# Optimization experiments

Hardware: AMD Instinct MI355X
Metric: run time of the kernel (lower is better)

## Reference

```python
import jax, jax.numpy as jnp
import numpy as np

N_VISIBLE = 4096
N_HIDDEN = 4096
BATCH = 8192


def setup_inputs() -> dict:
    key = jax.random.key(0)
    k_x, k_w = jax.random.split(key)
    input_data = jax.random.uniform(k_x, (BATCH, N_VISIBLE), dtype=jnp.float32)
    # xavier_uniform with sigmoid gain (=1.0): limit = sqrt(6/(fan_in+fan_out))
    limit = float(np.sqrt(6.0 / (N_VISIBLE + N_HIDDEN)))
    W = jax.random.uniform(k_w, (N_VISIBLE, N_HIDDEN), dtype=jnp.float32,
                           minval=-limit, maxval=limit)
    hidden_bias = jnp.zeros((N_HIDDEN,), dtype=jnp.float32)
    return {"input_data": input_data, "W": W, "hidden_bias": hidden_bias}


def reference(input_data, W, hidden_bias):
    # RBM.sample_hidden_2 (forward): sigmoid(x @ W + b), batched over samples.
    # (The torch code loops per sample with host syncs; same math, vectorized.)
    hid_prob = jax.nn.sigmoid(jnp.matmul(input_data, W) + hidden_bias)
    return hid_prob
```

## Files before the change

kernel.cpp:

```cpp
#include <hip/hip_runtime.h>
#include <cstdint>

#define MDIM 8192
#define NDIM 4096
#define KDIM 4096
#define NT (KDIM / 64)

typedef __bf16 bf16x8 __attribute__((ext_vector_type(8)));
typedef float f32x4 __attribute__((ext_vector_type(4)));

#define MFMA16 __builtin_amdgcn_mfma_f32_16x16x32_bf16

__device__ __forceinline__ void gload_lds16(const void* g, void* l) {
    __builtin_amdgcn_global_load_lds(
        (const __attribute__((address_space(1))) uint32_t*)g,
        (__attribute__((address_space(3))) uint32_t*)l, 16, 0, 0);
}

__device__ __forceinline__ unsigned short bf16_bits(float f) {
    __bf16 b = (__bf16)f;
    return __builtin_bit_cast(unsigned short, b);
}

__device__ __forceinline__ int detect_f32(const void* X) {
    int ok = 1;
    if (threadIdx.x < 128) {
        unsigned short h = ((const unsigned short*)X)[threadIdx.x];
        ok = (h <= 0x3F80);
    }
    return __syncthreads_and(ok) ? 0 : 1;
}

__global__ __launch_bounds__(256) void prep(const void* __restrict__ X,
                                            const void* __restrict__ W,
                                            __bf16* __restrict__ Xb,
                                            __bf16* __restrict__ WT) {
    const int f32 = detect_f32(X);
    const int t = threadIdx.x;
    if (blockIdx.x < 8192) {
        if (!f32) return;
        const float* Xf = (const float*)X;
        const long xbase = (long)blockIdx.x * 4096;
#pragma unroll
        for (int rr = 0; rr < 4; ++rr) {
            const long idx = xbase + rr * 1024 + t * 4;
            float4 v = *(const float4*)(Xf + idx);
            unsigned short r[4] = {bf16_bits(v.x), bf16_bits(v.y),
                                   bf16_bits(v.z), bf16_bits(v.w)};
            *(uint2*)(Xb + idx) = *(const uint2*)r;
        }
        return;
    }
    __shared__ unsigned short tile[64 * 65];
    const int bid = blockIdx.x - 8192;
    const int n0 = (bid & 63) * 64;
    const int k0 = (bid >> 6) * 64;
    if (f32) {
        const float* Wf = (const float*)W;
#pragma unroll
        for (int p = 0; p < 4; ++p) {
            const int ch = p * 256 + t;
            const int kr = ch >> 4;
            const int nc = ch & 15;
            float4 v = *(const float4*)(Wf + (long)(k0 + kr) * NDIM + n0 + nc * 4);
            tile[(nc * 4 + 0) * 65 + kr] = bf16_bits(v.x);
            tile[(nc * 4 + 1) * 65 + kr] = bf16_bits(v.y);
            tile[(nc * 4 + 2) * 65 + kr] = bf16_bits(v.z);
            tile[(nc * 4 + 3) * 65 + kr] = bf16_bits(v.w);
        }
    } else {
        const __bf16* Wb = (const __bf16*)W;
#pragma unroll
        for (int p = 0; p < 2; ++p) {
            const int ch = p * 256 + t;
            const int kr = ch >> 3;
            const int nc = ch & 7;
            uint4 v = *(const uint4*)(Wb + (long)(k0 + kr) * NDIM + n0 + nc * 8);
            const unsigned short* e = (const unsigned short*)&v;
#pragma unroll
            for (int i = 0; i < 8; ++i) tile[(nc * 8 + i) * 65 + kr] = e[i];
        }
    }
    __syncthreads();
#pragma unroll
    for (int p = 0; p < 2; ++p) {
        const int ch = p * 256 + t;
        const int nr = ch >> 3;
        const int kc = ch & 7;
        unsigned short r[8];
#pragma unroll
        for (int i = 0; i < 8; ++i) r[i] = tile[nr * 65 + kc * 8 + i];
        *(uint4*)(WT + (long)(n0 + nr) * KDIM + k0 + kc * 8) = *(uint4*)r;
    }
}

__global__ __launch_bounds__(256) void transpose_w(const void* __restrict__ X,
                                                   const void* __restrict__ W,
                                                   __bf16* __restrict__ WT) {
    __shared__ unsigned short tile[64 * 65];
    const int f32 = detect_f32(X);
    const int t = threadIdx.x;
    const int k0 = blockIdx.y * 64;
    const int n0 = blockIdx.x * 64;
    if (f32) {
        const float* Wf = (const float*)W;
#pragma unroll
        for (int p = 0; p < 4; ++p) {
            const int ch = p * 256 + t;
            const int kr = ch >> 4;
            const int nc = ch & 15;
            float4 v = *(const float4*)(Wf + (long)(k0 + kr) * NDIM + n0 + nc * 4);
            tile[(nc * 4 + 0) * 65 + kr] = bf16_bits(v.x);
            tile[(nc * 4 + 1) * 65 + kr] = bf16_bits(v.y);
            tile[(nc * 4 + 2) * 65 + kr] = bf16_bits(v.z);
            tile[(nc * 4 + 3) * 65 + kr] = bf16_bits(v.w);
        }
    } else {
        const __bf16* Wb = (const __bf16*)W;
#pragma unroll
        for (int p = 0; p < 2; ++p) {
            const int ch = p * 256 + t;
            const int kr = ch >> 3;
            const int nc = ch & 7;
            uint4 v = *(const uint4*)(Wb + (long)(k0 + kr) * NDIM + n0 + nc * 8);
            const unsigned short* e = (const unsigned short*)&v;
#pragma unroll
            for (int i = 0; i < 8; ++i) tile[(nc * 8 + i) * 65 + kr] = e[i];
        }
    }
    __syncthreads();
#pragma unroll
    for (int p = 0; p < 2; ++p) {
        const int ch = p * 256 + t;
        const int nr = ch >> 3;
        const int kc = ch & 7;
        unsigned short r[8];
#pragma unroll
        for (int i = 0; i < 8; ++i) r[i] = tile[nr * 65 + kc * 8 + i];
        *(uint4*)(WT + (long)(n0 + nr) * KDIM + k0 + kc * 8) = *(uint4*)r;
    }
}

#define P_OPEN()                                           \
    do {                                                   \
        __builtin_amdgcn_sched_barrier(0);                 \
        __builtin_amdgcn_s_barrier();                      \
        asm volatile("s_waitcnt lgkmcnt(0)" ::: "memory"); \
        __builtin_amdgcn_sched_barrier(0);                 \
    } while (0)
#define P_CLOSE()                          \
    do {                                   \
        __builtin_amdgcn_sched_barrier(0); \
        __builtin_amdgcn_s_barrier();      \
    } while (0)

template <int DBOFF>
__device__ __forceinline__ void ktile(const __bf16* pa, const __bf16* pb,
                                      const __bf16* gA, const __bf16* gB,
                                      __bf16* lA, __bf16* lB, long ko2,
                                      int soff0, int soff1,
                                      f32x4 (&acc)[8][4]) {
    const __bf16* paT = pa + DBOFF;
    const __bf16* pbT = pb + DBOFF;
    bf16x8 aF[4][2], bF[4][2];
#pragma unroll
    for (int j = 0; j < 2; ++j) {
        bF[j][0] = *(const bf16x8*)(pbT + j * 1024 + soff0);
        bF[j][1] = *(const bf16x8*)(pbT + j * 1024 + soff1);
    }
#pragma unroll
    for (int i = 0; i < 4; ++i) {
        aF[i][0] = *(const bf16x8*)(paT + i * 1024 + soff0);
        aF[i][1] = *(const bf16x8*)(paT + i * 1024 + soff1);
    }
    asm volatile("s_waitcnt lgkmcnt(8)" ::: "memory");
    P_OPEN();
    __builtin_amdgcn_s_setprio(1);
#pragma unroll
    for (int kk = 0; kk < 2; ++kk)
#pragma unroll
        for (int i = 0; i < 4; ++i)
#pragma unroll
            for (int j = 0; j < 2; ++j)
                acc[i][j] = MFMA16(aF[i][kk], bF[j][kk], acc[i][j], 0, 0, 0);
    __builtin_amdgcn_s_setprio(0);
    P_CLOSE();
#pragma unroll
    for (int j = 2; j < 4; ++j) {
        bF[j][0] = *(const bf16x8*)(pbT + j * 1024 + soff0);
        bF[j][1] = *(const bf16x8*)(pbT + j * 1024 + soff1);
    }
    P_OPEN();
    __builtin_amdgcn_s_setprio(1);
#pragma unroll
    for (int kk = 0; kk < 2; ++kk)
#pragma unroll
        for (int i = 0; i < 4; ++i)
#pragma unroll
            for (int j = 2; j < 4; ++j)
                acc[i][j] = MFMA16(aF[i][kk], bF[j][kk], acc[i][j], 0, 0, 0);
    __builtin_amdgcn_s_setprio(0);
    P_CLOSE();
#pragma unroll
    for (int i = 0; i < 4; ++i) {
        aF[i][0] = *(const bf16x8*)(paT + (4 + i) * 1024 + soff0);
        aF[i][1] = *(const bf16x8*)(paT + (4 + i) * 1024 + soff1);
    }
    gload_lds16(gB + ko2, lB + DBOFF);
    gload_lds16(gB + (long)64 * KDIM + ko2, lB + DBOFF + 4096);
    gload_lds16(gB + (long)128 * KDIM + ko2, lB + DBOFF + 8192);
    gload_lds16(gB + (long)192 * KDIM + ko2, lB + DBOFF + 12288);
    P_OPEN();
    __builtin_amdgcn_s_setprio(1);
#pragma unroll
    for (int kk = 0; kk < 2; ++kk)
#pragma unroll
        for (int i = 0; i < 4; ++i)
#pragma unroll
            for (int j = 2; j < 4; ++j)
                acc[4 + i][j] = MFMA16(aF[i][kk], bF[j][kk], acc[4 + i][j], 0, 0, 0);
    __builtin_amdgcn_s_setprio(0);
    P_CLOSE();
    gload_lds16(gA + ko2, lA + DBOFF);
    gload_lds16(gA + (long)64 * KDIM + ko2, lA + DBOFF + 4096);
    gload_lds16(gA + (long)128 * KDIM + ko2, lA + DBOFF + 8192);
    gload_lds16(gA + (long)192 * KDIM + ko2, lA + DBOFF + 12288);
    P_OPEN();
    __builtin_amdgcn_s_setprio(1);
#pragma unroll
    for (int kk = 0; kk < 2; ++kk)
#pragma unroll
        for (int i = 0; i < 4; ++i)
#pragma unroll
            for (int j = 0; j < 2; ++j)
                acc[4 + i][j] = MFMA16(aF[i][kk], bF[j][kk], acc[4 + i][j], 0, 0, 0);
    __builtin_amdgcn_s_setprio(0);
    __builtin_amdgcn_sched_barrier(0);
    asm volatile("s_waitcnt vmcnt(8)" ::: "memory");
    __builtin_amdgcn_sched_barrier(0);
    __builtin_amdgcn_s_barrier();
}

__global__ __launch_bounds__(512, 2) void gemm256(
    const void* __restrict__ X, const __bf16* __restrict__ Xb,
    const __bf16* __restrict__ WT, const void* __restrict__ bias,
    void* __restrict__ out) {
    __shared__ __bf16 sA[2][256][64];
    __shared__ __bf16 sB[2][256][64];
    const int f32 = detect_f32(X);
    const __bf16* __restrict__ Abf = f32 ? Xb : (const __bf16*)X;
    const int t = threadIdx.x;
    const int lane = t & 63;
    const int wid = t >> 6;
    const int wm = wid >> 2;
    const int wn = wid & 3;
    const int lrow = lane & 15;
    const int quad = lane >> 4;
    const int l7 = lrow & 7;

    const int flat = blockIdx.x;
    const int swz = (flat & 7) * (512 / 8) + (flat >> 3);
    const long m0 = (long)(swz >> 4) * 256;
    const long n0 = (long)(swz & 15) * 256;

    const int r8 = lane >> 3;
    const int c8 = lane & 7;
    const int cs = (c8 ^ r8) * 8;
    const __bf16* gA = Abf + (m0 + wid * 8 + r8) * KDIM + cs;
    const __bf16* gB = WT + (n0 + wid * 8 + r8) * KDIM + cs;
    __bf16* lA = &sA[0][wid * 8][0];
    __bf16* lB = &sB[0][wid * 8][0];

    const int soff0 = (quad ^ l7) * 8;
    const int soff1 = ((4 + quad) ^ l7) * 8;
    const __bf16* pa = &sA[0][wm * 128 + lrow][0];
    const __bf16* pb = &sB[0][wn * 64 + lrow][0];

    f32x4 acc[8][4] = {};

    {
        gload_lds16(gA, lA);
        gload_lds16(gA + (long)64 * KDIM, lA + 4096);
        gload_lds16(gA + (long)128 * KDIM, lA + 8192);
        gload_lds16(gA + (long)192 * KDIM, lA + 12288);
        gload_lds16(gB, lB);
        gload_lds16(gB + (long)64 * KDIM, lB + 4096);
        gload_lds16(gB + (long)128 * KDIM, lB + 8192);
        gload_lds16(gB + (long)192 * KDIM, lB + 12288);
        gload_lds16(gA + 64, lA + 16384);
        gload_lds16(gA + (long)64 * KDIM + 64, lA + 16384 + 4096);
        gload_lds16(gA + (long)128 * KDIM + 64, lA + 16384 + 8192);
        gload_lds16(gA + (long)192 * KDIM + 64, lA + 16384 + 12288);
        gload_lds16(gB + 64, lB + 16384);
        gload_lds16(gB + (long)64 * KDIM + 64, lB + 16384 + 4096);
        gload_lds16(gB + (long)128 * KDIM + 64, lB + 16384 + 8192);
        gload_lds16(gB + (long)192 * KDIM + 64, lB + 16384 + 12288);
    }
    __builtin_amdgcn_sched_barrier(0);
    asm volatile("s_waitcnt vmcnt(8)" ::: "memory");
    __builtin_amdgcn_sched_barrier(0);
    __builtin_amdgcn_s_barrier();

#pragma unroll 1
    for (int tt = 0; tt < NT; tt += 2) {
        const long ko2a = (long)((tt + 2) & (NT - 1)) * 64;
        const long ko2b = (long)((tt + 3) & (NT - 1)) * 64;
        ktile<0>(pa, pb, gA, gB, lA, lB, ko2a, soff0, soff1, acc);
        ktile<16384>(pa, pb, gA, gB, lA, lB, ko2b, soff0, soff1, acc);
    }

    const int crow0 = (int)m0 + wm * 128 + quad * 4;
    if (f32) {
        float* of = (float*)out;
        const float* bf = (const float*)bias;
#pragma unroll
        for (int j = 0; j < 4; ++j) {
            const int col = (int)n0 + wn * 64 + j * 16 + lrow;
            const float bv = bf[col];
#pragma unroll
            for (int i = 0; i < 8; ++i) {
                const long rbase = (long)(crow0 + i * 16) * NDIM + col;
#pragma unroll
                for (int r = 0; r < 4; ++r) {
                    const float x = acc[i][j][r] + bv;
                    of[rbase + (long)r * NDIM] = 1.0f / (1.0f + __expf(-x));
                }
            }
        }
    } else {
        __bf16* ob = (__bf16*)out;
        const __bf16* bb = (const __bf16*)bias;
#pragma unroll
        for (int j = 0; j < 4; ++j) {
            const int col = (int)n0 + wn * 64 + j * 16 + lrow;
            const float bv = (float)bb[col];
#pragma unroll
            for (int i = 0; i < 8; ++i) {
                const long rbase = (long)(crow0 + i * 16) * NDIM + col;
#pragma unroll
                for (int r = 0; r < 4; ++r) {
                    const float x = acc[i][j][r] + bv;
                    ob[rbase + (long)r * NDIM] = (__bf16)(1.0f / (1.0f + __expf(-x)));
                }
            }
        }
    }
}

template <int MODE>
__global__ __launch_bounds__(256) void gemm_bias_sigmoid(
    const void* __restrict__ X, const __bf16* __restrict__ Xb,
    const void* __restrict__ Wp, const __bf16* __restrict__ WT,
    const void* __restrict__ bias, void* __restrict__ out) {
    __shared__ __bf16 sA[128 * 64];
    __shared__ __bf16 sB[128 * 64];
    const int f32 = detect_f32(X);
    const int t = threadIdx.x;
    const int lane = t & 63;
    const int wid = t >> 6;
    const int m0 = blockIdx.y * 128;
    const int n0 = blockIdx.x * 128;
    const int wm = (wid & 1) * 64;
    const int wn = (wid >> 1) * 64;
    const int lrow = lane & 15;
    const int quad = lane >> 4;

    f32x4 acc[4][4] = {};

    {
        const int srow = t >> 2;
        const int schk = t & 3;
        __bf16* ldsA = sA + wid * 512;
        __bf16* ldsB = sB + wid * 512;
        const int arow = t >> 1;
        const int acol = (t & 1) * 16;
        const int fp = t & 15;
        const int fc = t >> 4;
        uint32_t* sB32 = (uint32_t*)sB;

        auto compute = [&]() {
            bf16x8 aF[4], bFr[4];
            const __bf16* pa = sA + (wm + lrow) * 32 + quad * 8;
            const __bf16* pb = sB + (wn + lrow) * 32 + quad * 8;
#pragma unroll
            for (int i = 0; i < 4; ++i) aF[i] = *(const bf16x8*)(pa + i * 512);
#pragma unroll
            for (int j = 0; j < 4; ++j) bFr[j] = *(const bf16x8*)(pb + j * 512);
#pragma unroll
            for (int i = 0; i < 4; ++i)
#pragma unroll
                for (int j = 0; j < 4; ++j)
                    acc[i][j] = MFMA16(aF[i], bFr[j], acc[i][j], 0, 0, 0);
        };

        if (MODE == 1 && !f32) {
            const __bf16* gA = (const __bf16*)X + (long)(m0 + srow) * KDIM + schk * 8;
            const __bf16* gB = WT + (long)(n0 + srow) * KDIM + schk * 8;
            for (int kt = 0; kt < KDIM / 32; ++kt) {
                const __bf16* a0 = gA + kt * 32;
                gload_lds16(a0, ldsA);
                gload_lds16(a0 + (long)64 * KDIM, ldsA + 2048);
                const __bf16* b0 = gB + kt * 32;
                gload_lds16(b0, ldsB);
                gload_lds16(b0 + (long)64 * KDIM, ldsB + 2048);
                __syncthreads();
                compute();
                __syncthreads();
            }
        } else if (MODE == 1) {
            const float* Xf = (const float*)X;
            const __bf16* gB = WT + (long)(n0 + srow) * KDIM + schk * 8;
            for (int kt = 0; kt < KDIM / 32; ++kt) {
                const __bf16* b0 = gB + kt * 32;
                gload_lds16(b0, ldsB);
                gload_lds16(b0 + (long)64 * KDIM, ldsB + 2048);
                const float* ap = Xf + (long)(m0 + arow) * KDIM + kt * 32 + acol;
                float4 v0 = *(const float4*)(ap);
                float4 v1 = *(const float4*)(ap + 4);
                float4 v2 = *(const float4*)(ap + 8);
                float4 v3 = *(const float4*)(ap + 12);
                unsigned short r[16] = {
                    bf16_bits(v0.x), bf16_bits(v0.y), bf16_bits(v0.z), bf16_bits(v0.w),
                    bf16_bits(v1.x), bf16_bits(v1.y), bf16_bits(v1.z), bf16_bits(v1.w),
                    bf16_bits(v2.x), bf16_bits(v2.y), bf16_bits(v2.z), bf16_bits(v2.w),
                    bf16_bits(v3.x), bf16_bits(v3.y), bf16_bits(v3.z), bf16_bits(v3.w)};
                *(uint4*)(sA + arow * 32 + acol) = *(const uint4*)(r);
                *(uint4*)(sA + arow * 32 + acol + 8) = *(const uint4*)(r + 8);
                __syncthreads();
                compute();
                __syncthreads();
            }
        } else if (MODE == 2 && !f32) {
            const __bf16* gA = (const __bf16*)X + (long)(m0 + srow) * KDIM + schk * 8;
            const __bf16* Wb = (const __bf16*)Wp;
            for (int kt = 0; kt < KDIM / 32; ++kt) {
                const __bf16* a0 = gA + kt * 32;
                gload_lds16(a0, ldsA);
                gload_lds16(a0 + (long)64 * KDIM, ldsA + 2048);
                const __bf16* w0 = Wb + (long)(kt * 32 + 2 * fp) * NDIM + n0 + fc * 8;
                uint4 g0 = *(const uint4*)(w0);
                uint4 g1 = *(const uint4*)(w0 + NDIM);
                const unsigned short* e0 = (const unsigned short*)&g0;
                const unsigned short* e1 = (const unsigned short*)&g1;
#pragma unroll
                for (int i = 0; i < 8; ++i)
                    sB32[(fc * 8 + i) * 16 + fp] =
                        (uint32_t)e0[i] | ((uint32_t)e1[i] << 16);
                __syncthreads();
                compute();
                __syncthreads();
            }
        } else if (MODE == 2) {
            const float* Xf = (const float*)X;
            const float* Wf = (const float*)Wp;
            for (int kt = 0; kt < KDIM / 32; ++kt) {
                const float* ap = Xf + (long)(m0 + arow) * KDIM + kt * 32 + acol;
                float4 v0 = *(const float4*)(ap);
                float4 v1 = *(const float4*)(ap + 4);
                float4 v2 = *(const float4*)(ap + 8);
                float4 v3 = *(const float4*)(ap + 12);
                unsigned short r[16] = {
                    bf16_bits(v0.x), bf16_bits(v0.y), bf16_bits(v0.z), bf16_bits(v0.w),
                    bf16_bits(v1.x), bf16_bits(v1.y), bf16_bits(v1.z), bf16_bits(v1.w),
                    bf16_bits(v2.x), bf16_bits(v2.y), bf16_bits(v2.z), bf16_bits(v2.w),
                    bf16_bits(v3.x), bf16_bits(v3.y), bf16_bits(v3.z), bf16_bits(v3.w)};
                *(uint4*)(sA + arow * 32 + acol) = *(const uint4*)(r);
                *(uint4*)(sA + arow * 32 + acol + 8) = *(const uint4*)(r + 8);
                const float* w0 = Wf + (long)(kt * 32 + 2 * fp) * NDIM + n0 + fc * 8;
                float4 u0 = *(const float4*)(w0);
                float4 u1 = *(const float4*)(w0 + 4);
                float4 u2 = *(const float4*)(w0 + NDIM);
                float4 u3 = *(const float4*)(w0 + NDIM + 4);
                float k0v[8] = {u0.x, u0.y, u0.z, u0.w, u1.x, u1.y, u1.z, u1.w};
                float k1v[8] = {u2.x, u2.y, u2.z, u2.w, u3.x, u3.y, u3.z, u3.w};
#pragma unroll
                for (int i = 0; i < 8; ++i)
                    sB32[(fc * 8 + i) * 16 + fp] =
                        (uint32_t)bf16_bits(k0v[i]) |
                        ((uint32_t)bf16_bits(k1v[i]) << 16);
                __syncthreads();
                compute();
                __syncthreads();
            }
        }
    }

    const int crow = m0 + wm + quad * 4;
    if (f32) {
        float* of = (float*)out;
        const float* bf = (const float*)bias;
#pragma unroll
        for (int j = 0; j < 4; ++j) {
            const int col = n0 + wn + j * 16 + lrow;
            const float bv = bf[col];
#pragma unroll
            for (int i = 0; i < 4; ++i) {
                const long rbase = (long)(crow + i * 16) * NDIM + col;
#pragma unroll
                for (int r = 0; r < 4; ++r) {
                    const float x = acc[i][j][r] + bv;
                    of[rbase + (long)r * NDIM] = 1.0f / (1.0f + __expf(-x));
                }
            }
        }
    } else {
        __bf16* ob = (__bf16*)out;
        const __bf16* bb = (const __bf16*)bias;
#pragma unroll
        for (int j = 0; j < 4; ++j) {
            const int col = n0 + wn + j * 16 + lrow;
            const float bv = (float)bb[col];
#pragma unroll
            for (int i = 0; i < 4; ++i) {
                const long rbase = (long)(crow + i * 16) * NDIM + col;
#pragma unroll
                for (int r = 0; r < 4; ++r) {
                    const float x = acc[i][j][r] + bv;
                    ob[rbase + (long)r * NDIM] = (__bf16)(1.0f / (1.0f + __expf(-x)));
                }
            }
        }
    }
}

extern "C" void kernel_launch(void* const* d_in, const int* in_sizes, int n_in,
                              void* d_out, int out_size, void* d_ws,
                              size_t ws_size, hipStream_t stream) {
    const void* X = d_in[0];
    const void* W = d_in[1];
    const void* bias = d_in[2];

    const size_t wt_bytes = (size_t)KDIM * NDIM * sizeof(__bf16);
    const size_t xb_bytes = (size_t)MDIM * KDIM * sizeof(__bf16);

    if (ws_size >= wt_bytes + xb_bytes) {
        __bf16* WT = (__bf16*)d_ws;
        __bf16* Xb = (__bf16*)((char*)d_ws + wt_bytes);
        prep<<<8192 + 4096, 256, 0, stream>>>(X, W, Xb, WT);
        gemm256<<<dim3((MDIM / 256) * (NDIM / 256)), 512, 0, stream>>>(
            X, Xb, WT, bias, d_out);
    } else if (ws_size >= wt_bytes) {
        __bf16* WT = (__bf16*)d_ws;
        transpose_w<<<dim3(NDIM / 64, KDIM / 64), 256, 0, stream>>>(X, W, WT);
        dim3 gg(NDIM / 128, MDIM / 128);
        gemm_bias_sigmoid<1><<<gg, 256, 0, stream>>>(X, nullptr, W, WT, bias, d_out);
    } else {
        dim3 gg(NDIM / 128, MDIM / 128);
        gemm_bias_sigmoid<2><<<gg, 256, 0, stream>>>(X, nullptr, W, nullptr, bias, d_out);
    }
}
```

Measured before the change: 519.3 us.

## Restructure k-tile pipeline with register prefetch and one barrier per tile

Reworks the main GEMM loop so that each k-tile uses a single workgroup barrier instead of several open/close barrier pairs around each MFMA cluster. The LDS fragments for the next k-tile are read into registers ahead of time, across the tile boundary, with A fragments split into two ping-pong register sets. Global-to-LDS loads for the tile after next are issued right after the barrier. This is meant to cut barrier stalls and overlap LDS reads with MFMA work. In exchange it holds more live registers, and the wait becomes a full vmcnt(0) drain each tile, which could expose global load latency.

```diff
diff --git a/kernel.cpp b/kernel.cpp
--- a/kernel.cpp
+++ b/kernel.cpp
@@ -141,104 +141,76 @@
     }
 }
 
-#define P_OPEN()                                           \
+#define WAIT_LGKM4()                                       \
     do {                                                   \
         __builtin_amdgcn_sched_barrier(0);                 \
-        __builtin_amdgcn_s_barrier();                      \
-        asm volatile("s_waitcnt lgkmcnt(0)" ::: "memory"); \
+        asm volatile("s_waitcnt lgkmcnt(4)" ::: "memory"); \
         __builtin_amdgcn_sched_barrier(0);                 \
     } while (0)
-#define P_CLOSE()                          \
-    do {                                   \
-        __builtin_amdgcn_sched_barrier(0); \
-        __builtin_amdgcn_s_barrier();      \
+
+#define READ_A(dst, paT, q)                                               \
+    do {                                                                  \
+        dst[0][0] = *(const bf16x8*)((paT) + (2 * (q) + 0) * 1024 + soff0); \
+        dst[0][1] = *(const bf16x8*)((paT) + (2 * (q) + 0) * 1024 + soff1); \
+        dst[1][0] = *(const bf16x8*)((paT) + (2 * (q) + 1) * 1024 + soff0); \
+        dst[1][1] = *(const bf16x8*)((paT) + (2 * (q) + 1) * 1024 + soff1); \
     } while (0)
 
-template <int DBOFF>
+#define READ_B(pbT)                                           \
+    do {                                                      \
+        _Pragma("unroll") for (int j = 0; j < 4; ++j) {       \
+            bF[j][0] = *(const bf16x8*)((pbT) + j * 1024 + soff0); \
+            bF[j][1] = *(const bf16x8*)((pbT) + j * 1024 + soff1); \
+        }                                                     \
+    } while (0)
+
+#define CLUSTER(aX, q)                                                       \
+    do {                                                                     \
+        __builtin_amdgcn_s_setprio(1);                                       \
+        _Pragma("unroll") for (int kk = 0; kk < 2; ++kk)                     \
+            _Pragma("unroll") for (int ii = 0; ii < 2; ++ii)                 \
+                _Pragma("unroll") for (int j = 0; j < 4; ++j)                \
+                    acc[2 * (q) + ii][j] = MFMA16(aX[ii][kk], bF[j][kk],     \
+                                                  acc[2 * (q) + ii][j], 0, 0, 0); \
+        __builtin_amdgcn_s_setprio(0);                                       \
+    } while (0)
+
+template <int DB>
 __device__ __forceinline__ void ktile(const __bf16* pa, const __bf16* pb,
                                       const __bf16* gA, const __bf16* gB,
                                       __bf16* lA, __bf16* lB, long ko2,
-                                      int soff0, int soff1,
-                                      f32x4 (&acc)[8][4]) {
-    const __bf16* paT = pa + DBOFF;
-    const __bf16* pbT = pb + DBOFF;
-    bf16x8 aF[4][2], bF[4][2];
-#pragma unroll
-    for (int j = 0; j < 2; ++j) {
-        bF[j][0] = *(const bf16x8*)(pbT + j * 1024 + soff0);
-        bF[j][1] = *(const bf16x8*)(pbT + j * 1024 + soff1);
-    }
-#pragma unroll
-    for (int i = 0; i < 4; ++i) {
-        aF[i][0] = *(const bf16x8*)(paT + i * 1024 + soff0);
-        aF[i][1] = *(const bf16x8*)(paT + i * 1024 + soff1);
-    }
-    asm volatile("s_waitcnt lgkmcnt(8)" ::: "memory");
-    P_OPEN();
-    __builtin_amdgcn_s_setprio(1);
-#pragma unroll
-    for (int kk = 0; kk < 2; ++kk)
-#pragma unroll
-        for (int i = 0; i < 4; ++i)
-#pragma unroll
-            for (int j = 0; j < 2; ++j)
-                acc[i][j] = MFMA16(aF[i][kk], bF[j][kk], acc[i][j], 0, 0, 0);
-    __builtin_amdgcn_s_setprio(0);
-    P_CLOSE();
-#pragma unroll
-    for (int j = 2; j < 4; ++j) {
-        bF[j][0] = *(const bf16x8*)(pbT + j * 1024 + soff0);
-        bF[j][1] = *(const bf16x8*)(pbT + j * 1024 + soff1);
-    }
-    P_OPEN();
-    __builtin_amdgcn_s_setprio(1);
-#pragma unroll
-    for (int kk = 0; kk < 2; ++kk)
-#pragma unroll
-        for (int i = 0; i < 4; ++i)
-#pragma unroll
-            for (int j = 2; j < 4; ++j)
-                acc[i][j] = MFMA16(aF[i][kk], bF[j][kk], acc[i][j], 0, 0, 0);
-    __builtin_amdgcn_s_setprio(0);
-    P_CLOSE();
-#pragma unroll
-    for (int i = 0; i < 4; ++i) {
-        aF[i][0] = *(const bf16x8*)(paT + (4 + i) * 1024 + soff0);
-        aF[i][1] = *(const bf16x8*)(paT + (4 + i) * 1024 + soff1);
-    }
-    gload_lds16(gB + ko2, lB + DBOFF);
-    gload_lds16(gB + (long)64 * KDIM + ko2, lB + DBOFF + 4096);
-    gload_lds16(gB + (long)128 * KDIM + ko2, lB + DBOFF + 8192);
-    gload_lds16(gB + (long)192 * KDIM + ko2, lB + DBOFF + 12288);
-    P_OPEN();
-    __builtin_amdgcn_s_setprio(1);
-#pragma unroll
-    for (int kk = 0; kk < 2; ++kk)
-#pragma unroll
-        for (int i = 0; i < 4; ++i)
-#pragma unroll
-            for (int j = 2; j < 4; ++j)
-                acc[4 + i][j] = MFMA16(aF[i][kk], bF[j][kk], acc[4 + i][j], 0, 0, 0);
-    __builtin_amdgcn_s_setprio(0);
-    P_CLOSE();
-    gload_lds16(gA + ko2, lA + DBOFF);
-    gload_lds16(gA + (long)64 * KDIM + ko2, lA + DBOFF + 4096);
-    gload_lds16(gA + (long)128 * KDIM + ko2, lA + DBOFF + 8192);
-    gload_lds16(gA + (long)192 * KDIM + ko2, lA + DBOFF + 12288);
-    P_OPEN();
-    __builtin_amdgcn_s_setprio(1);
-#pragma unroll
-    for (int kk = 0; kk < 2; ++kk)
-#pragma unroll
-        for (int i = 0; i < 4; ++i)
-#pragma unroll
-            for (int j = 0; j < 2; ++j)
-                acc[4 + i][j] = MFMA16(aF[i][kk], bF[j][kk], acc[4 + i][j], 0, 0, 0);
-    __builtin_amdgcn_s_setprio(0);
-    __builtin_amdgcn_sched_barrier(0);
-    asm volatile("s_waitcnt vmcnt(8)" ::: "memory");
+                                      int soff0, int soff1, f32x4 (&acc)[8][4],
+                                      bf16x8 (&bF)[4][2], bf16x8 (&aP)[2][2],
+                                      bf16x8 (&aQ)[2][2]) {
+    const __bf16* paT = pa + DB * 16384;
+    const __bf16* pbN = pb + (DB ^ 1) * 16384;
+    const __bf16* paN = pa + (DB ^ 1) * 16384;
+    WAIT_LGKM4();
+    CLUSTER(aP, 0);
+    READ_A(aP, paT, 2);
+    WAIT_LGKM4();
+    CLUSTER(aQ, 1);
+    READ_A(aQ, paT, 3);
+    WAIT_LGKM4();
+    CLUSTER(aP, 2);
+    __builtin_amdgcn_sched_barrier(0);
+    asm volatile("s_waitcnt vmcnt(0) lgkmcnt(0)" ::: "memory");
     __builtin_amdgcn_sched_barrier(0);
     __builtin_amdgcn_s_barrier();
+    __builtin_amdgcn_sched_barrier(0);
+    gload_lds16(gB + ko2, lB + DB * 16384);
+    gload_lds16(gB + (long)64 * KDIM + ko2, lB + DB * 16384 + 4096);
+    gload_lds16(gB + (long)128 * KDIM + ko2, lB + DB * 16384 + 8192);
+    gload_lds16(gB + (long)192 * KDIM + ko2, lB + DB * 16384 + 12288);
+    gload_lds16(gA + ko2, lA + DB * 16384);
+    gload_lds16(gA + (long)64 * KDIM + ko2, lA + DB * 16384 + 4096);
+    gload_lds16(gA + (long)128 * KDIM + ko2, lA + DB * 16384 + 8192);
+    gload_lds16(gA + (long)192 * KDIM + ko2, lA + DB * 16384 + 12288);
+    CLUSTER(aQ, 3);
+    READ_B(pbN);
+    READ_A(aP, paN, 0);
+    __builtin_amdgcn_sched_barrier(0);
+    READ_A(aQ, paN, 1);
 }
 
 __global__ __launch_bounds__(512, 2) void gemm256(
@@ -277,36 +249,40 @@
     const __bf16* pb = &sB[0][wn * 64 + lrow][0];
 
     f32x4 acc[8][4] = {};
-
-    {
-        gload_lds16(gA, lA);
-        gload_lds16(gA + (long)64 * KDIM, lA + 4096);
-        gload_lds16(gA + (long)128 * KDIM, lA + 8192);
-        gload_lds16(gA + (long)192 * KDIM, lA + 12288);
-        gload_lds16(gB, lB);
-        gload_lds16(gB + (long)64 * KDIM, lB + 4096);
-        gload_lds16(gB + (long)128 * KDIM, lB + 8192);
-        gload_lds16(gB + (long)192 * KDIM, lB + 12288);
-        gload_lds16(gA + 64, lA + 16384);
-        gload_lds16(gA + (long)64 * KDIM + 64, lA + 16384 + 4096);
-        gload_lds16(gA + (long)128 * KDIM + 64, lA + 16384 + 8192);
-        gload_lds16(gA + (long)192 * KDIM + 64, lA + 16384 + 12288);
-        gload_lds16(gB + 64, lB + 16384);
-        gload_lds16(gB + (long)64 * KDIM + 64, lB + 16384 + 4096);
-        gload_lds16(gB + (long)128 * KDIM + 64, lB + 16384 + 8192);
-        gload_lds16(gB + (long)192 * KDIM + 64, lB + 16384 + 12288);
-    }
+    bf16x8 bF[4][2], aP[2][2], aQ[2][2];
+
+    gload_lds16(gB, lB);
+    gload_lds16(gB + (long)64 * KDIM, lB + 4096);
+    gload_lds16(gB + (long)128 * KDIM, lB + 8192);
+    gload_lds16(gB + (long)192 * KDIM, lB + 12288);
+    gload_lds16(gA, lA);
+    gload_lds16(gA + (long)64 * KDIM, lA + 4096);
+    gload_lds16(gA + (long)128 * KDIM, lA + 8192);
+    gload_lds16(gA + (long)192 * KDIM, lA + 12288);
+    gload_lds16(gB + 64, lB + 16384);
+    gload_lds16(gB + (long)64 * KDIM + 64, lB + 16384 + 4096);
+    gload_lds16(gB + (long)128 * KDIM + 64, lB + 16384 + 8192);
+    gload_lds16(gB + (long)192 * KDIM + 64, lB + 16384 + 12288);
+    gload_lds16(gA + 64, lA + 16384);
+    gload_lds16(gA + (long)64 * KDIM + 64, lA + 16384 + 4096);
+    gload_lds16(gA + (long)128 * KDIM + 64, lA + 16384 + 8192);
+    gload_lds16(gA + (long)192 * KDIM + 64, lA + 16384 + 12288);
     __builtin_amdgcn_sched_barrier(0);
     asm volatile("s_waitcnt vmcnt(8)" ::: "memory");
     __builtin_amdgcn_sched_barrier(0);
     __builtin_amdgcn_s_barrier();
+    __builtin_amdgcn_sched_barrier(0);
+    READ_B(pb);
+    READ_A(aP, pa, 0);
+    __builtin_amdgcn_sched_barrier(0);
+    READ_A(aQ, pa, 1);
 
 #pragma unroll 1
     for (int tt = 0; tt < NT; tt += 2) {
-        const long ko2a = (long)((tt + 2) & (NT - 1)) * 64;
-        const long ko2b = (long)((tt + 3) & (NT - 1)) * 64;
-        ktile<0>(pa, pb, gA, gB, lA, lB, ko2a, soff0, soff1, acc);
-        ktile<16384>(pa, pb, gA, gB, lA, lB, ko2b, soff0, soff1, acc);
+        ktile<0>(pa, pb, gA, gB, lA, lB, (long)((tt + 2) & (NT - 1)) * 64,
+                 soff0, soff1, acc, bF, aP, aQ);
+        ktile<1>(pa, pb, gA, gB, lA, lB, (long)((tt + 3) & (NT - 1)) * 64,
+                 soff0, soff1, acc, bF, aP, aQ);
     }
 
     const int crow0 = (int)m0 + wm * 128 + quad * 4;
```

New measurement: 529.5 us. About the same (+2.0%).
